# Kernel tuning notes

Hardware: AMD Instinct MI355X
Metric: run time of the kernel (lower is better)

Reference implementation:

```python
import jax, jax.numpy as jnp
import numpy as np

N_IN, N_HID, N_OUT = 2048, 4096, 1024
N_TOT = N_IN + N_HID + N_OUT
BATCH = 4096


def _structure_mask():
    # input -> {hidden, output}; hidden -> {hidden, output}; nothing feeds inputs,
    # outputs feed nothing.
    m = np.zeros((N_TOT, N_TOT), dtype=np.float32)
    m[0:N_IN, N_IN:N_TOT] = 1.0
    m[N_IN:N_IN + N_HID, N_IN:N_TOT] = 1.0
    return jnp.asarray(m)


def setup_inputs() -> dict:
    key = jax.random.key(0)
    kx, kw = jax.random.split(key)
    x = jax.random.normal(kx, (BATCH, N_IN), dtype=jnp.float32)
    weights = jax.random.normal(kw, (N_TOT, N_TOT), dtype=jnp.float32) * 0.1
    structure_mask = _structure_mask()
    return {"x": x, "weights": weights, "structure_mask": structure_mask}


def reference(x, weights, structure_mask):
    # Faithful to the torch forward: the per-neuron hidden loop reads the
    # activation vector BEFORE any hidden value is written, so every hidden
    # unit sees only [x, 0, 0]; outputs then see [x, hidden, 0].
    Wm = weights * structure_mask  # (N_TOT, N_TOT)
    B = x.shape[0]
    a0 = jnp.concatenate(
        [x, jnp.zeros((B, N_HID + N_OUT), dtype=x.dtype)], axis=1)  # (B, N_TOT)
    hidden = jax.nn.relu(a0 @ Wm[:, N_IN:N_IN + N_HID])             # (B, N_HID)
    a1 = jnp.concatenate(
        [x, hidden, jnp.zeros((B, N_OUT), dtype=x.dtype)], axis=1)  # (B, N_TOT)
    out = a1 @ Wm[:, N_IN + N_HID:]                                 # (B, N_OUT)
    return out
```

## Files before the change

### kernel.cpp

```cpp
#include <hip/hip_runtime.h>
#include <hip/hip_bf16.h>

#define N_IN  2048
#define N_HID 4096
#define N_OUT 1024
#define N_TOT 7168
#define BATCH 4096
#define LDA2  (N_IN + N_HID)

typedef __attribute__((ext_vector_type(8))) short short8;
typedef __attribute__((ext_vector_type(4))) float f32x4;

static __device__ __forceinline__ unsigned short f2bf(float f) {
  __hip_bfloat16 h = __float2bfloat16(f);
  return __builtin_bit_cast(unsigned short, h);
}

__global__ void conv_x_kernel(const float* __restrict__ x,
                              unsigned short* __restrict__ A2) {
  int idx = blockIdx.x * 256 + threadIdx.x;
  int row = idx >> 9;
  int col = (idx & 511) << 2;
  const float4 v = *(const float4*)(x + (size_t)row * N_IN + col);
  ushort4 o;
  o.x = f2bf(v.x); o.y = f2bf(v.y); o.z = f2bf(v.z); o.w = f2bf(v.w);
  *(ushort4*)(A2 + (size_t)row * LDA2 + col) = o;
}

__global__ void conv_t_kernel(const float* __restrict__ src, int lds_,
                              unsigned short* __restrict__ dst, int ldd,
                              int SK, int SN) {
  __shared__ float tile[32][33];
  const int t = threadIdx.x;
  const int k0 = blockIdx.y << 5, n0 = blockIdx.x << 5;
  const int r = t >> 3, c = (t & 7) << 2;
  const float4 v = *(const float4*)(src + (size_t)(k0 + r) * lds_ + n0 + c);
  tile[r][c] = v.x; tile[r][c + 1] = v.y; tile[r][c + 2] = v.z; tile[r][c + 3] = v.w;
  __syncthreads();
  ushort4 o;
  o.x = f2bf(tile[c][r]);
  o.y = f2bf(tile[c + 1][r]);
  o.z = f2bf(tile[c + 2][r]);
  o.w = f2bf(tile[c + 3][r]);
  *(ushort4*)(dst + (size_t)(n0 + r) * ldd + k0 + c) = o;
}

template <int WMODE>
__global__ __launch_bounds__(256)
void gemm_bt(const unsigned short* __restrict__ A, int lda,
             const unsigned short* __restrict__ Bt, int ldb,
             void* __restrict__ Cv, int ldc, int Klen) {
  __shared__ __align__(16) unsigned short As[128 * 64];
  __shared__ __align__(16) unsigned short Bs[128 * 64];

  const int tid  = threadIdx.x;
  const int lane = tid & 63;
  const int wave = tid >> 6;
  const int wy = wave >> 1, wx = wave & 1;
  const int lm = lane & 15, quad = lane >> 4;
  const int bm = blockIdx.y, bn = blockIdx.x;
  const int ko0 = blockIdx.z * Klen;

  const int grow = (wave << 5) + (lane >> 3);
  const int gcol = ((lane & 7) ^ (lane >> 3)) << 3;

  const unsigned short* Ag = A  + (size_t)(bm * 128 + grow) * lda + gcol + ko0;
  const unsigned short* Bg = Bt + (size_t)(bn * 128 + grow) * ldb + gcol + ko0;
  unsigned short* Asl = As + wave * 2048;
  unsigned short* Bsl = Bs + wave * 2048;

  f32x4 acc[4][4];
#pragma unroll
  for (int i = 0; i < 4; ++i)
#pragma unroll
    for (int j = 0; j < 4; ++j)
      acc[i][j] = (f32x4){0.f, 0.f, 0.f, 0.f};

  for (int ko = 0; ko < Klen; ko += 64) {
    __syncthreads();
#pragma unroll
    for (int i = 0; i < 4; ++i) {
      __builtin_amdgcn_global_load_lds(
          (const __attribute__((address_space(1))) void*)(Ag + (size_t)(8 * i) * lda + ko),
          (__attribute__((address_space(3))) void*)(Asl + i * 512), 16, 0, 0);
      __builtin_amdgcn_global_load_lds(
          (const __attribute__((address_space(1))) void*)(Bg + (size_t)(8 * i) * ldb + ko),
          (__attribute__((address_space(3))) void*)(Bsl + i * 512), 16, 0, 0);
    }
    __syncthreads();

#pragma unroll
    for (int kk = 0; kk < 2; ++kk) {
      short8 av[4], bv[4];
#pragma unroll
      for (int mt = 0; mt < 4; ++mt) {
        const int r = wy * 64 + mt * 16 + lm;
        av[mt] = *(const short8*)(As + r * 64 + (((kk * 4 + quad) ^ (lm & 7)) << 3));
      }
#pragma unroll
      for (int nt = 0; nt < 4; ++nt) {
        const int r = wx * 64 + nt * 16 + lm;
        bv[nt] = *(const short8*)(Bs + r * 64 + (((kk * 4 + quad) ^ (lm & 7)) << 3));
      }
#pragma unroll
      for (int mt = 0; mt < 4; ++mt)
#pragma unroll
        for (int nt = 0; nt < 4; ++nt)
          acc[mt][nt] = __builtin_amdgcn_mfma_f32_16x16x32_bf16(
              av[mt], bv[nt], acc[mt][nt], 0, 0, 0);
    }
  }

  if (WMODE == 1) {
    unsigned short* C = (unsigned short*)Cv;
#pragma unroll
    for (int mt = 0; mt < 4; ++mt) {
      const int row0 = bm * 128 + wy * 64 + mt * 16 + quad * 4;
#pragma unroll
      for (int nt = 0; nt < 4; ++nt) {
        const int col = bn * 128 + wx * 64 + nt * 16 + lm;
#pragma unroll
        for (int r = 0; r < 4; ++r) {
          float v = acc[mt][nt][r];
          v = v > 0.f ? v : 0.f;
          C[(size_t)(row0 + r) * ldc + col] = f2bf(v);
        }
      }
    }
  } else if (WMODE == 0) {
    float* C = (float*)Cv;
#pragma unroll
    for (int mt = 0; mt < 4; ++mt) {
      const int row0 = bm * 128 + wy * 64 + mt * 16 + quad * 4;
#pragma unroll
      for (int nt = 0; nt < 4; ++nt) {
        const int col = bn * 128 + wx * 64 + nt * 16 + lm;
#pragma unroll
        for (int r = 0; r < 4; ++r)
          C[(size_t)(row0 + r) * ldc + col] = acc[mt][nt][r];
      }
    }
  } else {
    float* C = (float*)Cv;
#pragma unroll
    for (int mt = 0; mt < 4; ++mt) {
      const int row0 = bm * 128 + wy * 64 + mt * 16 + quad * 4;
#pragma unroll
      for (int nt = 0; nt < 4; ++nt) {
        const int col = bn * 128 + wx * 64 + nt * 16 + lm;
#pragma unroll
        for (int r = 0; r < 4; ++r)
          atomicAdd(&C[(size_t)(row0 + r) * ldc + col], acc[mt][nt][r]);
      }
    }
  }
}

extern "C" void kernel_launch(void* const* d_in, const int* in_sizes, int n_in,
                              void* d_out, int out_size, void* d_ws, size_t ws_size,
                              hipStream_t stream) {
  const float* x = (const float*)d_in[0];
  const float* W = (const float*)d_in[1];

  char* ws = (char*)d_ws;
  const size_t A2_BYTES  = (size_t)BATCH * LDA2 * 2;
  const size_t BT1_BYTES = (size_t)N_HID * N_IN * 2;
  unsigned short* A2  = (unsigned short*)ws;
  unsigned short* Bt1 = (unsigned short*)(ws + A2_BYTES);
  unsigned short* Bt2 = (unsigned short*)(ws + A2_BYTES + BT1_BYTES);

  hipMemsetAsync(d_out, 0, (size_t)out_size * sizeof(float), stream);

  conv_x_kernel<<<(BATCH * N_IN / 4) / 256, 256, 0, stream>>>(x, A2);

  conv_t_kernel<<<dim3(N_HID / 32, N_IN / 32), 256, 0, stream>>>(
      W + N_IN, N_TOT, Bt1, N_IN, N_IN, N_HID);

  conv_t_kernel<<<dim3(N_OUT / 32, LDA2 / 32), 256, 0, stream>>>(
      W + N_IN + N_HID, N_TOT, Bt2, LDA2, LDA2, N_OUT);

  gemm_bt<1><<<dim3(N_HID / 128, BATCH / 128), 256, 0, stream>>>(
      A2, LDA2, Bt1, N_IN, A2 + N_IN, LDA2, N_IN);

  gemm_bt<2><<<dim3(N_OUT / 128, BATCH / 128, 2), 256, 0, stream>>>(
      A2, LDA2, Bt2, LDA2, d_out, N_OUT, LDA2 / 2);
}
```

Measured before the change: 518.0 us.

## Stage GEMM epilogues through LDS and replace atomic split-K with partial buffers

The GEMM epilogues now write their results into shared memory and then store them with coalesced 16-byte vector writes. The previous path used scattered scalar stores or per-element atomics. The second GEMM's split-K factor goes from 2 to 4, and each split writes its own fp32 partial buffer in the workspace. A separate kernel then sums the four partials into the output, so the memset and the atomics are no longer needed. This adds a reduction pass and 64 MB of partial-buffer traffic, and it relies on the workspace having room for the partials.

```diff
diff --git a/kernel.cpp b/kernel.cpp
--- a/kernel.cpp
+++ b/kernel.cpp
@@ -7,6 +7,7 @@
 #define N_TOT 7168
 #define BATCH 4096
 #define LDA2  (N_IN + N_HID)
+#define OUT_ELEMS ((size_t)BATCH * N_OUT)
 
 typedef __attribute__((ext_vector_type(8))) short short8;
 typedef __attribute__((ext_vector_type(4))) float f32x4;
@@ -45,13 +46,28 @@
   *(ushort4*)(dst + (size_t)(n0 + r) * ldd + k0 + c) = o;
 }
 
+__global__ void add4_kernel(const float* __restrict__ P, float* __restrict__ out) {
+  size_t i = ((size_t)blockIdx.x * 256 + threadIdx.x) * 4;
+  float4 a = *(const float4*)(P + i);
+  float4 b = *(const float4*)(P + OUT_ELEMS + i);
+  float4 c = *(const float4*)(P + 2 * OUT_ELEMS + i);
+  float4 d = *(const float4*)(P + 3 * OUT_ELEMS + i);
+  float4 o;
+  o.x = (a.x + b.x) + (c.x + d.x);
+  o.y = (a.y + b.y) + (c.y + d.y);
+  o.z = (a.z + b.z) + (c.z + d.z);
+  o.w = (a.w + b.w) + (c.w + d.w);
+  *(float4*)(out + i) = o;
+}
+
 template <int WMODE>
 __global__ __launch_bounds__(256)
 void gemm_bt(const unsigned short* __restrict__ A, int lda,
              const unsigned short* __restrict__ Bt, int ldb,
-             void* __restrict__ Cv, int ldc, int Klen) {
-  __shared__ __align__(16) unsigned short As[128 * 64];
-  __shared__ __align__(16) unsigned short Bs[128 * 64];
+             void* __restrict__ Cv, int ldc, int Klen, size_t zstride) {
+  __shared__ __align__(16) char smem[34816];
+  unsigned short* As = (unsigned short*)smem;
+  unsigned short* Bs = (unsigned short*)(smem + 16384);
 
   const int tid  = threadIdx.x;
   const int lane = tid & 63;
@@ -111,47 +127,59 @@
     }
   }
 
+  __syncthreads();
+
   if (WMODE == 1) {
-    unsigned short* C = (unsigned short*)Cv;
+    unsigned short* Cs = (unsigned short*)smem;
 #pragma unroll
     for (int mt = 0; mt < 4; ++mt) {
-      const int row0 = bm * 128 + wy * 64 + mt * 16 + quad * 4;
+      const int row0 = wy * 64 + mt * 16 + quad * 4;
 #pragma unroll
       for (int nt = 0; nt < 4; ++nt) {
-        const int col = bn * 128 + wx * 64 + nt * 16 + lm;
+        const int col = wx * 64 + nt * 16 + lm;
 #pragma unroll
         for (int r = 0; r < 4; ++r) {
           float v = acc[mt][nt][r];
-          v = v > 0.f ? v : 0.f;
-          C[(size_t)(row0 + r) * ldc + col] = f2bf(v);
+          Cs[(row0 + r) * 136 + col] = f2bf(v > 0.f ? v : 0.f);
         }
       }
     }
-  } else if (WMODE == 0) {
-    float* C = (float*)Cv;
-#pragma unroll
-    for (int mt = 0; mt < 4; ++mt) {
-      const int row0 = bm * 128 + wy * 64 + mt * 16 + quad * 4;
-#pragma unroll
-      for (int nt = 0; nt < 4; ++nt) {
-        const int col = bn * 128 + wx * 64 + nt * 16 + lm;
-#pragma unroll
-        for (int r = 0; r < 4; ++r)
-          C[(size_t)(row0 + r) * ldc + col] = acc[mt][nt][r];
-      }
+    __syncthreads();
+    unsigned short* C = (unsigned short*)Cv;
+    const int col = (tid & 15) << 3;
+#pragma unroll
+    for (int i = 0; i < 8; ++i) {
+      const int row = (tid >> 4) + 16 * i;
+      short8 v = *(const short8*)(Cs + row * 136 + col);
+      *(short8*)(C + (size_t)(bm * 128 + row) * ldc + bn * 128 + col) = v;
     }
   } else {
-    float* C = (float*)Cv;
-#pragma unroll
-    for (int mt = 0; mt < 4; ++mt) {
-      const int row0 = bm * 128 + wy * 64 + mt * 16 + quad * 4;
-#pragma unroll
-      for (int nt = 0; nt < 4; ++nt) {
-        const int col = bn * 128 + wx * 64 + nt * 16 + lm;
-#pragma unroll
-        for (int r = 0; r < 4; ++r)
-          atomicAdd(&C[(size_t)(row0 + r) * ldc + col], acc[mt][nt][r]);
-      }
+    float* Csf = (float*)smem;
+    float* C = (float*)Cv + (size_t)blockIdx.z * zstride;
+#pragma unroll
+    for (int p = 0; p < 2; ++p) {
+      if (wy == p) {
+#pragma unroll
+        for (int mt = 0; mt < 4; ++mt) {
+          const int row0 = mt * 16 + quad * 4;
+#pragma unroll
+          for (int nt = 0; nt < 4; ++nt) {
+            const int col = wx * 64 + nt * 16 + lm;
+#pragma unroll
+            for (int r = 0; r < 4; ++r)
+              Csf[(row0 + r) * 132 + col] = acc[mt][nt][r];
+          }
+        }
+      }
+      __syncthreads();
+      const int col = (tid & 31) << 2;
+#pragma unroll
+      for (int i = 0; i < 8; ++i) {
+        const int row = (tid >> 5) + 8 * i;
+        float4 v = *(const float4*)(Csf + row * 132 + col);
+        *(float4*)(C + (size_t)(bm * 128 + p * 64 + row) * ldc + bn * 128 + col) = v;
+      }
+      if (p == 0) __syncthreads();
     }
   }
 }
@@ -165,11 +193,11 @@
   char* ws = (char*)d_ws;
   const size_t A2_BYTES  = (size_t)BATCH * LDA2 * 2;
   const size_t BT1_BYTES = (size_t)N_HID * N_IN * 2;
+  const size_t BT2_BYTES = (size_t)N_OUT * LDA2 * 2;
   unsigned short* A2  = (unsigned short*)ws;
   unsigned short* Bt1 = (unsigned short*)(ws + A2_BYTES);
   unsigned short* Bt2 = (unsigned short*)(ws + A2_BYTES + BT1_BYTES);
-
-  hipMemsetAsync(d_out, 0, (size_t)out_size * sizeof(float), stream);
+  float*          P   = (float*)(ws + A2_BYTES + BT1_BYTES + BT2_BYTES);
 
   conv_x_kernel<<<(BATCH * N_IN / 4) / 256, 256, 0, stream>>>(x, A2);
 
@@ -180,8 +208,10 @@
       W + N_IN + N_HID, N_TOT, Bt2, LDA2, LDA2, N_OUT);
 
   gemm_bt<1><<<dim3(N_HID / 128, BATCH / 128), 256, 0, stream>>>(
-      A2, LDA2, Bt1, N_IN, A2 + N_IN, LDA2, N_IN);
-
-  gemm_bt<2><<<dim3(N_OUT / 128, BATCH / 128, 2), 256, 0, stream>>>(
-      A2, LDA2, Bt2, LDA2, d_out, N_OUT, LDA2 / 2);
-}
+      A2, LDA2, Bt1, N_IN, A2 + N_IN, LDA2, N_IN, 0);
+
+  gemm_bt<0><<<dim3(N_OUT / 128, BATCH / 128, 4), 256, 0, stream>>>(
+      A2, LDA2, Bt2, LDA2, P, N_OUT, LDA2 / 4, OUT_ELEMS);
+
+  add4_kernel<<<(OUT_ELEMS / 4) / 256, 256, 0, stream>>>(P, (float*)d_out);
+}
```

After: 523.8 us. About the same (+1.1%).
